# Kernel optimization log

Measured on AMD Instinct MI355X. Metric: run time of the kernel, lower is better.

## Reference

```python
import jax, jax.numpy as jnp
import numpy as np

N = 16384

def setup_inputs() -> dict:
    key = jax.random.key(0)
    k1, k2, k3 = jax.random.split(key, 3)
    risk_scores = jax.random.normal(k1, (N,), dtype=jnp.float32)
    survival_times = jax.random.normal(k2, (N,), dtype=jnp.float32)
    # 0/1 event indicator (1 = event observed, 0 = censored)
    events = (jax.random.uniform(k3, (N,)) < 0.5).astype(jnp.float32)
    return {"risk_scores": risk_scores, "survival_times": survival_times, "events": events}

def reference(risk_scores, survival_times, events):
    # Risk-set matrix: R[i, j] = 1 if T[j] >= T[i] (vectorized version of the
    # original O(n^2) double Python loop).
    R = (survival_times[None, :] >= survival_times[:, None]).astype(risk_scores.dtype)  # [n, n]
    exp_theta = jnp.exp(risk_scores)                # [n]
    # sum_j exp(theta_j) * R[i, j]  ->  matvec
    risk_set_sum = R @ exp_theta                    # [n]
    loss = -jnp.mean((risk_scores - jnp.log(risk_set_sum)) * events)
    return loss
```

## Files before the change

### kernel.cpp

```cpp
#include <hip/hip_runtime.h>
#include <math.h>

#define BLOCK 256
#define KB_ 16384
#define SCAN_T 1024

__global__ void surv_hist(const float* __restrict__ theta,
                          const float* __restrict__ T,
                          int* __restrict__ counts, float* __restrict__ bucketE,
                          float* __restrict__ Earr, int* __restrict__ elemB,
                          int* __restrict__ elemR, int n) {
    int i = blockIdx.x * BLOCK + threadIdx.x;
    if (i >= n) return;
    float Tg = T[i];
    float E  = expf(theta[i]);
    int b = (int)((Tg + 6.0f) * (KB_ / 12.0f));
    b = min(max(b, 0), KB_ - 1);
    int r = atomicAdd(&counts[b], 1);
    atomicAdd(&bucketE[b], E);
    Earr[i] = E; elemB[i] = b; elemR[i] = r;
}

__global__ void surv_scan(const int* __restrict__ counts,
                          const float* __restrict__ bucketE,
                          int* __restrict__ offsets, float* __restrict__ suffixE,
                          int n) {
    __shared__ int   ci[SCAN_T];
    __shared__ float ce[SCAN_T];
    const int t = threadIdx.x;
    const int chunk = KB_ / SCAN_T;
    const int base = t * chunk;
    int cs = 0; float es = 0.f;
    for (int k = 0; k < chunk; ++k) { cs += counts[base + k]; es += bucketE[base + k]; }
    ci[t] = cs; ce[t] = es;
    __syncthreads();
    for (int s = 1; s < SCAN_T; s <<= 1) {
        int   a = (t >= s)          ? ci[t - s] : 0;
        float f = (t + s < SCAN_T)  ? ce[t + s] : 0.f;
        __syncthreads();
        ci[t] += a; ce[t] += f;
        __syncthreads();
    }
    int run = ci[t] - cs;
    for (int k = 0; k < chunk; ++k) { offsets[base + k] = run; run += counts[base + k]; }
    float rs = ce[t] - es;
    for (int k = chunk - 1; k >= 0; --k) { rs += bucketE[base + k]; suffixE[base + k] = rs; }
    if (t == 0) { offsets[KB_] = n; suffixE[KB_] = 0.f; }
}

__global__ void surv_scatter(const float* __restrict__ T, const float* __restrict__ Earr,
                             const int* __restrict__ elemB, const int* __restrict__ elemR,
                             const int* __restrict__ offsets,
                             float* __restrict__ sortedT, float* __restrict__ sortedE, int n) {
    int i = blockIdx.x * BLOCK + threadIdx.x;
    if (i >= n) return;
    int b = elemB[i];
    int pos = offsets[b] + elemR[i];
    sortedT[pos] = T[i];
    sortedE[pos] = Earr[i];
}

__global__ void surv_risk(const float* __restrict__ theta, const float* __restrict__ T,
                          const float* __restrict__ events,
                          const int* __restrict__ elemB, const int* __restrict__ offsets,
                          const float* __restrict__ suffixE,
                          const float* __restrict__ sortedT, const float* __restrict__ sortedE,
                          float* __restrict__ bsum, int n) {
    __shared__ float red[BLOCK];
    const int tid = threadIdx.x;
    const int i = blockIdx.x * BLOCK + tid;
    float term = 0.f;
    if (i < n) {
        int b = elemB[i];
        float Ti = T[i];
        float risk = suffixE[b + 1];
        const int p0 = offsets[b], p1 = offsets[b + 1];
        for (int p = p0; p < p1; ++p)
            risk += (sortedT[p] >= Ti) ? sortedE[p] : 0.f;
        term = (theta[i] - logf(risk)) * events[i];
    }
    red[tid] = term;
    __syncthreads();
    for (int s = BLOCK / 2; s > 0; s >>= 1) {
        if (tid < s) red[tid] += red[tid + s];
        __syncthreads();
    }
    if (tid == 0) bsum[blockIdx.x] = red[0];
}

__global__ void surv_final(const float* __restrict__ bsum, float* __restrict__ out,
                           int nblocks, int n) {
    float v = 0.f;
    for (int b = threadIdx.x; b < nblocks; b += 64) v += bsum[b];
    for (int off = 32; off > 0; off >>= 1) v += __shfl_down(v, off, 64);
    if (threadIdx.x == 0) out[0] = -v / (float)n;
}

__global__ void surv_partial_bf(const float* __restrict__ theta, const float* __restrict__ T,
                                const float* __restrict__ events, float* __restrict__ bsum, int n) {
    __shared__ float red[BLOCK];
    const int tid = threadIdx.x;
    const int i = blockIdx.x * BLOCK + tid;
    float term = 0.f;
    if (i < n) {
        const float Ti = T[i];
        float risk = 0.f;
        for (int j = 0; j < n; ++j)
            risk += (T[j] >= Ti) ? expf(theta[j]) : 0.f;
        term = (theta[i] - logf(risk)) * events[i];
    }
    red[tid] = term;
    __syncthreads();
    for (int s = BLOCK / 2; s > 0; s >>= 1) {
        if (tid < s) red[tid] += red[tid + s];
        __syncthreads();
    }
    if (tid == 0) bsum[blockIdx.x] = red[0];
}

extern "C" void kernel_launch(void* const* d_in, const int* in_sizes, int n_in,
                              void* d_out, int out_size, void* d_ws, size_t ws_size,
                              hipStream_t stream) {
    const float* theta  = (const float*)d_in[0];
    const float* T      = (const float*)d_in[1];
    const float* events = (const float*)d_in[2];
    float* out = (float*)d_out;
    const int n = in_sizes[0];
    const int nbi = (n + BLOCK - 1) / BLOCK;

    const size_t need = ((size_t)2 * KB_ + 2 * (KB_ + 1) + 5 * (size_t)n + nbi) * 4;

    if ((size_t)ws_size < need) {
        float* bsum = (float*)d_ws;
        surv_partial_bf<<<nbi, BLOCK, 0, stream>>>(theta, T, events, bsum, n);
        surv_final<<<1, 64, 0, stream>>>(bsum, out, nbi, n);
        return;
    }

    int*   counts  = (int*)d_ws;
    float* bucketE = (float*)(counts + KB_);
    int*   offsets = (int*)(bucketE + KB_);
    float* suffixE = (float*)(offsets + KB_ + 1);
    float* sortedT = suffixE + KB_ + 1;
    float* sortedE = sortedT + n;
    float* Earr    = sortedE + n;
    int*   elemB   = (int*)(Earr + n);
    int*   elemR   = elemB + n;
    float* bsum    = (float*)(elemR + n);

    hipMemsetAsync(d_ws, 0, (size_t)2 * KB_ * 4, stream);
    surv_hist<<<nbi, BLOCK, 0, stream>>>(theta, T, counts, bucketE, Earr, elemB, elemR, n);
    surv_scan<<<1, SCAN_T, 0, stream>>>(counts, bucketE, offsets, suffixE, n);
    surv_scatter<<<nbi, BLOCK, 0, stream>>>(T, Earr, elemB, elemR, offsets, sortedT, sortedE, n);
    surv_risk<<<nbi, BLOCK, 0, stream>>>(theta, T, events, elemB, offsets, suffixE,
                                         sortedT, sortedE, bsum, n);
    surv_final<<<1, 64, 0, stream>>>(bsum, out, nbi, n);
}
```

Before: 80.91 us.

## Replace bucket-sort pipeline with brute-force pairwise risk sum and single-pass reduction

```diff
diff --git a/kernel.cpp b/kernel.cpp
--- a/kernel.cpp
+++ b/kernel.cpp
@@ -1,99 +1,71 @@
 #include <hip/hip_runtime.h>
 #include <math.h>
 
+#define PBLOCK 256
+#define MT 1024
+#define NSLICE 16
 #define BLOCK 256
-#define KB_ 16384
-#define SCAN_T 1024
 
-__global__ void surv_hist(const float* __restrict__ theta,
+__global__ void surv_prep(const float* __restrict__ theta,
                           const float* __restrict__ T,
-                          int* __restrict__ counts, float* __restrict__ bucketE,
-                          float* __restrict__ Earr, int* __restrict__ elemB,
-                          int* __restrict__ elemR, int n) {
-    int i = blockIdx.x * BLOCK + threadIdx.x;
-    if (i >= n) return;
-    float Tg = T[i];
-    float E  = expf(theta[i]);
-    int b = (int)((Tg + 6.0f) * (KB_ / 12.0f));
-    b = min(max(b, 0), KB_ - 1);
-    int r = atomicAdd(&counts[b], 1);
-    atomicAdd(&bucketE[b], E);
-    Earr[i] = E; elemB[i] = b; elemR[i] = r;
+                          float2* __restrict__ PE,
+                          float* __restrict__ accum, int* __restrict__ ticket,
+                          int n) {
+    int i = blockIdx.x * PBLOCK + threadIdx.x;
+    if (i == 0) { *accum = 0.f; *ticket = 0; }
+    if (i < n) {
+        PE[i] = make_float2(T[i], expf(theta[i]));
+    }
 }
 
-__global__ void surv_scan(const int* __restrict__ counts,
-                          const float* __restrict__ bucketE,
-                          int* __restrict__ offsets, float* __restrict__ suffixE,
-                          int n) {
-    __shared__ int   ci[SCAN_T];
-    __shared__ float ce[SCAN_T];
-    const int t = threadIdx.x;
-    const int chunk = KB_ / SCAN_T;
-    const int base = t * chunk;
-    int cs = 0; float es = 0.f;
-    for (int k = 0; k < chunk; ++k) { cs += counts[base + k]; es += bucketE[base + k]; }
-    ci[t] = cs; ce[t] = es;
+__global__ __launch_bounds__(MT) void surv_main(
+        const float* __restrict__ theta, const float* __restrict__ T,
+        const float* __restrict__ events, const float2* __restrict__ PE,
+        float* __restrict__ accum, int* __restrict__ ticket,
+        float* __restrict__ out, int n) {
+    __shared__ float part[NSLICE][64];
+    const int tid  = threadIdx.x;
+    const int w    = __builtin_amdgcn_readfirstlane(tid >> 6);
+    const int lane = tid & 63;
+    const int i    = blockIdx.x * 64 + lane;
+    const float Ti = T[i];
+
+    const int slice = n / NSLICE;
+    const int nq    = slice >> 1;
+    const float4* __restrict__ PE4 = (const float4*)PE;
+    const int q0 = (w * slice) >> 1;
+
+    float r0 = 0.f, r1 = 0.f, r2 = 0.f, r3 = 0.f;
+    #pragma unroll 4
+    for (int q = 0; q < nq; q += 2) {
+        float4 a = PE4[q0 + q];
+        float4 b = PE4[q0 + q + 1];
+        r0 += (a.x >= Ti) ? a.y : 0.f;
+        r1 += (a.z >= Ti) ? a.w : 0.f;
+        r2 += (b.x >= Ti) ? b.y : 0.f;
+        r3 += (b.z >= Ti) ? b.w : 0.f;
+    }
+    part[w][lane] = (r0 + r1) + (r2 + r3);
     __syncthreads();
-    for (int s = 1; s < SCAN_T; s <<= 1) {
-        int   a = (t >= s)          ? ci[t - s] : 0;
-        float f = (t + s < SCAN_T)  ? ce[t + s] : 0.f;
-        __syncthreads();
-        ci[t] += a; ce[t] += f;
-        __syncthreads();
+
+    if (w == 0) {
+        float risk = part[0][lane];
+        #pragma unroll
+        for (int ww = 1; ww < NSLICE; ++ww) risk += part[ww][lane];
+        float term = (theta[i] - logf(risk)) * events[i];
+        #pragma unroll
+        for (int off = 32; off > 0; off >>= 1)
+            term += __shfl_down(term, off, 64);
+        if (lane == 0) {
+            atomicAdd(accum, term);
+            __threadfence();
+            int t = atomicAdd(ticket, 1);
+            if (t == (int)gridDim.x - 1) {
+                float tot = atomicAdd(accum, 0.0f);
+                out[0] = -tot / (float)n;
+            }
+        }
     }
-    int run = ci[t] - cs;
-    for (int k = 0; k < chunk; ++k) { offsets[base + k] = run; run += counts[base + k]; }
-    float rs = ce[t] - es;
-    for (int k = chunk - 1; k >= 0; --k) { rs += bucketE[base + k]; suffixE[base + k] = rs; }
-    if (t == 0) { offsets[KB_] = n; suffixE[KB_] = 0.f; }
-}
-
-__global__ void surv_scatter(const float* __restrict__ T, const float* __restrict__ Earr,
-                             const int* __restrict__ elemB, const int* __restrict__ elemR,
-                             const int* __restrict__ offsets,
-                             float* __restrict__ sortedT, float* __restrict__ sortedE, int n) {
-    int i = blockIdx.x * BLOCK + threadIdx.x;
-    if (i >= n) return;
-    int b = elemB[i];
-    int pos = offsets[b] + elemR[i];
-    sortedT[pos] = T[i];
-    sortedE[pos] = Earr[i];
-}
-
-__global__ void surv_risk(const float* __restrict__ theta, const float* __restrict__ T,
-                          const float* __restrict__ events,
-                          const int* __restrict__ elemB, const int* __restrict__ offsets,
-                          const float* __restrict__ suffixE,
-                          const float* __restrict__ sortedT, const float* __restrict__ sortedE,
-                          float* __restrict__ bsum, int n) {
-    __shared__ float red[BLOCK];
-    const int tid = threadIdx.x;
-    const int i = blockIdx.x * BLOCK + tid;
-    float term = 0.f;
-    if (i < n) {
-        int b = elemB[i];
-        float Ti = T[i];
-        float risk = suffixE[b + 1];
-        const int p0 = offsets[b], p1 = offsets[b + 1];
-        for (int p = p0; p < p1; ++p)
-            risk += (sortedT[p] >= Ti) ? sortedE[p] : 0.f;
-        term = (theta[i] - logf(risk)) * events[i];
-    }
-    red[tid] = term;
-    __syncthreads();
-    for (int s = BLOCK / 2; s > 0; s >>= 1) {
-        if (tid < s) red[tid] += red[tid + s];
-        __syncthreads();
-    }
-    if (tid == 0) bsum[blockIdx.x] = red[0];
-}
-
-__global__ void surv_final(const float* __restrict__ bsum, float* __restrict__ out,
-                           int nblocks, int n) {
-    float v = 0.f;
-    for (int b = threadIdx.x; b < nblocks; b += 64) v += bsum[b];
-    for (int off = 32; off > 0; off >>= 1) v += __shfl_down(v, off, 64);
-    if (threadIdx.x == 0) out[0] = -v / (float)n;
 }
 
 __global__ void surv_partial_bf(const float* __restrict__ theta, const float* __restrict__ T,
@@ -118,6 +90,14 @@
     if (tid == 0) bsum[blockIdx.x] = red[0];
 }
 
+__global__ void surv_final(const float* __restrict__ bsum, float* __restrict__ out,
+                           int nblocks, int n) {
+    float v = 0.f;
+    for (int b = threadIdx.x; b < nblocks; b += 64) v += bsum[b];
+    for (int off = 32; off > 0; off >>= 1) v += __shfl_down(v, off, 64);
+    if (threadIdx.x == 0) out[0] = -v / (float)n;
+}
+
 extern "C" void kernel_launch(void* const* d_in, const int* in_sizes, int n_in,
                               void* d_out, int out_size, void* d_ws, size_t ws_size,
                               hipStream_t stream) {
@@ -126,33 +106,25 @@
     const float* events = (const float*)d_in[2];
     float* out = (float*)d_out;
     const int n = in_sizes[0];
-    const int nbi = (n + BLOCK - 1) / BLOCK;
 
-    const size_t need = ((size_t)2 * KB_ + 2 * (KB_ + 1) + 5 * (size_t)n + nbi) * 4;
+    const size_t need = (size_t)n * 8 + 256;
+    const bool fast = (n > 0) && (n % 1024 == 0) && ((size_t)ws_size >= need);
 
-    if ((size_t)ws_size < need) {
+    if (!fast) {
+        const int nbi = (n + BLOCK - 1) / BLOCK;
         float* bsum = (float*)d_ws;
         surv_partial_bf<<<nbi, BLOCK, 0, stream>>>(theta, T, events, bsum, n);
         surv_final<<<1, 64, 0, stream>>>(bsum, out, nbi, n);
         return;
     }
 
-    int*   counts  = (int*)d_ws;
-    float* bucketE = (float*)(counts + KB_);
-    int*   offsets = (int*)(bucketE + KB_);
-    float* suffixE = (float*)(offsets + KB_ + 1);
-    float* sortedT = suffixE + KB_ + 1;
-    float* sortedE = sortedT + n;
-    float* Earr    = sortedE + n;
-    int*   elemB   = (int*)(Earr + n);
-    int*   elemR   = elemB + n;
-    float* bsum    = (float*)(elemR + n);
+    float2* PE     = (float2*)d_ws;
+    float*  accum  = (float*)(PE + n);
+    int*    ticket = (int*)(accum + 1);
 
-    hipMemsetAsync(d_ws, 0, (size_t)2 * KB_ * 4, stream);
-    surv_hist<<<nbi, BLOCK, 0, stream>>>(theta, T, counts, bucketE, Earr, elemB, elemR, n);
-    surv_scan<<<1, SCAN_T, 0, stream>>>(counts, bucketE, offsets, suffixE, n);
-    surv_scatter<<<nbi, BLOCK, 0, stream>>>(T, Earr, elemB, elemR, offsets, sortedT, sortedE, n);
-    surv_risk<<<nbi, BLOCK, 0, stream>>>(theta, T, events, elemB, offsets, suffixE,
-                                         sortedT, sortedE, bsum, n);
-    surv_final<<<1, 64, 0, stream>>>(bsum, out, nbi, n);
+    const int pb = (n + PBLOCK - 1) / PBLOCK;
+    const int mb = n / 64;
+
+    surv_prep<<<pb, PBLOCK, 0, stream>>>(theta, T, PE, accum, ticket, n);
+    surv_main<<<mb, MT, 0, stream>>>(theta, T, events, PE, accum, ticket, out, n);
 }
```

Measured after the change: 99.03 us. +22.4%, slower.
